# Performance work log

Hardware: AMD Instinct MI355X
Metric: run time of the kernel (lower is better)

Reference implementation:

```python
import jax, jax.numpy as jnp
import numpy as np

H = 8
D_MODEL = 1024
D_K = D_MODEL // H
NEG = -1000000000.0


def layer_norm(x, a, b, eps=1e-06):
    # torch std: unbiased (ddof=1); module divides by (std + eps)
    mean = jnp.mean(x, axis=-1, keepdims=True)
    var = jnp.sum((x - mean) ** 2, axis=-1, keepdims=True) / (x.shape[-1] - 1)
    std = jnp.sqrt(var)
    return a * (x - mean) / (std + eps) + b


def setup_inputs() -> dict:
    key = jax.random.key(0)
    ks = jax.random.split(key, 12)
    B, S, D = 8, 1024, D_MODEL
    inp = {
        "query": jax.random.normal(ks[0], (B, S, D), jnp.float32),
        "value": jax.random.normal(ks[1], (B, S, D), jnp.float32),
        "key": jax.random.normal(ks[2], (B, S, D), jnp.float32),
        "mask": jax.random.randint(ks[3], (B, S), 0, 2, jnp.int32),
        "ln_a": jnp.ones((D,), jnp.float32),
        "ln_b": jnp.zeros((D,), jnp.float32),
        "wq": jax.random.normal(ks[4], (D, D), jnp.float32) * 0.02,
        "bq": jnp.zeros((D,), jnp.float32),
        "wk": jax.random.normal(ks[5], (D, D), jnp.float32) * 0.02,
        "bk": jnp.zeros((D,), jnp.float32),
        "wv": jax.random.normal(ks[6], (D, D), jnp.float32) * 0.02,
        "bv": jnp.zeros((D,), jnp.float32),
        "w_aoa": jax.random.normal(ks[7], (2 * D, 2 * D), jnp.float32) * 0.02,  # [out, in]
        "b_aoa": jnp.zeros((2 * D,), jnp.float32),
    }
    return inp


def reference(query, value, key, mask, ln_a, ln_b, wq, bq, wk, bk, wv, bv, w_aoa, b_aoa):
    B, S, D = query.shape
    # mask [B,S] -> [B,1,1,S]
    m = mask[:, None, None, :]
    # norm_q
    q = layer_norm(query, ln_a, ln_b)
    # QKV projections, split heads -> [B,H,S,Dk]
    def split_heads(x):
        return x.reshape(B, -1, H, D_K).transpose(0, 2, 1, 3)
    q_ = split_heads(q @ wq.T + bq)
    k_ = split_heads(key @ wk.T + bk)
    v_ = split_heads(value @ wv.T + bv)
    scores = jnp.einsum("bhqd,bhkd->bhqk", q_, k_) / jnp.sqrt(jnp.float32(D_K))
    scores = jnp.where(m == 0, NEG, scores)
    p = jax.nn.softmax(scores, axis=-1)
    x = jnp.einsum("bhqk,bhkd->bhqd", p, v_)
    x = x.transpose(0, 2, 1, 3).reshape(B, S, D)
    # AoA: concat with (normed) query, linear to 2D, GLU
    z = jnp.concatenate([x, q], axis=-1) @ w_aoa.T + b_aoa
    a, g = jnp.split(z, 2, axis=-1)
    return a * jax.nn.sigmoid(g)
```

## Files before the change

kernel.cpp:

```cpp
#include <hip/hip_runtime.h>

typedef __attribute__((ext_vector_type(8))) __bf16 bf16x8;
typedef __attribute__((ext_vector_type(4))) float f32x4;
typedef __attribute__((ext_vector_type(16))) float f32x16;
typedef __attribute__((ext_vector_type(2))) int i32x2;

__device__ __forceinline__ ushort f2b(float f) {
    uint u = __builtin_bit_cast(uint, f);
    u += 0x7fffu + ((u >> 16) & 1u);
    return (ushort)(u >> 16);
}
__device__ __forceinline__ float b2f(ushort h) {
    uint u = ((uint)h) << 16;
    return __builtin_bit_cast(float, u);
}
__device__ __forceinline__ uint cvtpk(float a, float b) {
    uint r;
    asm("v_cvt_pk_bf16_f32 %0, %1, %2" : "=v"(r) : "v"(a), "v"(b));
    return r;
}

__global__ __launch_bounds__(256) void cast_kernel(const float* __restrict__ src,
                                                   ushort* __restrict__ dst) {
    size_t i = ((size_t)blockIdx.x * 256 + threadIdx.x) * 4;
    float4 v = *(const float4*)(src + i);
    ushort4 o;
    o.x = f2b(v.x); o.y = f2b(v.y); o.z = f2b(v.z); o.w = f2b(v.w);
    *(ushort4*)(dst + i) = o;
}

__global__ __launch_bounds__(256) void cast_permute_aoa(const float* __restrict__ src,
                                                        ushort* __restrict__ dst) {
    int n1 = blockIdx.x >> 1;
    int c = (blockIdx.x & 1) * 1024 + threadIdx.x * 4;
    int q = ((n1 & 63) | ((n1 >> 7) << 6)) + ((n1 >> 6) & 1) * 1024;
    float4 v = *(const float4*)(src + (size_t)q * 2048 + c);
    ushort4 o;
    o.x = f2b(v.x); o.y = f2b(v.y); o.z = f2b(v.z); o.w = f2b(v.w);
    *(ushort4*)(dst + (size_t)n1 * 2048 + c) = o;
}

__global__ __launch_bounds__(256) void ln_kernel(const float* __restrict__ x,
                                                 const float* __restrict__ ga,
                                                 const float* __restrict__ be,
                                                 ushort* __restrict__ xq) {
    const int row = blockIdx.x, tid = threadIdx.x;
    __shared__ float red[4];
    float4 v = ((const float4*)(x + (size_t)row * 1024))[tid];
    float sm = v.x + v.y + v.z + v.w;
    for (int off = 32; off; off >>= 1) sm += __shfl_xor(sm, off);
    if ((tid & 63) == 0) red[tid >> 6] = sm;
    __syncthreads();
    float mean = (red[0] + red[1] + red[2] + red[3]) * (1.f / 1024.f);
    __syncthreads();
    float dx = v.x - mean, dy = v.y - mean, dz = v.z - mean, dw = v.w - mean;
    float s2 = dx * dx + dy * dy + dz * dz + dw * dw;
    for (int off = 32; off; off >>= 1) s2 += __shfl_xor(s2, off);
    if ((tid & 63) == 0) red[tid >> 6] = s2;
    __syncthreads();
    float var = (red[0] + red[1] + red[2] + red[3]) * (1.f / 1023.f);
    float inv = 1.f / (sqrtf(var) + 1e-6f);
    float4 g = ((const float4*)ga)[tid];
    float4 bb = ((const float4*)be)[tid];
    ushort4 o;
    o.x = f2b(g.x * dx * inv + bb.x);
    o.y = f2b(g.y * dy * inv + bb.y);
    o.z = f2b(g.z * dz * inv + bb.z);
    o.w = f2b(g.w * dw * inv + bb.w);
    *(ushort4*)&xq[(size_t)row * 2048 + 1024 + tid * 4] = o;
}

template <int MODE>
__global__ __launch_bounds__(512, 2) void gemm6(const ushort* __restrict__ Aq, int ldaq,
                                                const ushort* __restrict__ Ak,
                                                const ushort* __restrict__ Av,
                                                const ushort* __restrict__ B, int ldb,
                                                const float* __restrict__ bias0,
                                                const float* __restrict__ bias1,
                                                const float* __restrict__ bias2,
                                                void* __restrict__ out0,
                                                void* __restrict__ out1,
                                                void* __restrict__ out2,
                                                int K, int NB, float qscale) {
    __shared__ ushort lds[2][32768];

    const int tid = threadIdx.x;
    const int w = tid >> 6, l = tid & 63;
    const int wr = w >> 2, wcn = w & 3;
    const int r16 = l & 15, g4 = l >> 4;

    const int bid = blockIdx.x;
    const int cpx = gridDim.x >> 3;
    const int swz = (bid & 7) * cpx + (bid >> 3);
    const int m0 = (swz / NB) * 256;
    const int n0 = (swz % NB) * 256;

    const int region = (MODE == 0) ? (n0 >> 10) : 0;
    const ushort* A = (MODE == 0) ? (region == 0 ? Aq : (region == 1 ? Ak : Av)) : Aq;
    const int lda = (MODE == 0) ? (region == 0 ? ldaq : 1024) : ldaq;

    const int srow8 = l >> 3;
    const int sxor8 = ((l & 7) ^ srow8) * 8;
    const ushort* As0 = A + (size_t)(m0 + w * 8 + srow8) * lda + sxor8;
    const ushort* Bs0 = B + (size_t)(n0 + w * 8 + srow8) * ldb + sxor8;

    f32x4 acc[8][4];
#pragma unroll
    for (int i = 0; i < 8; i++)
#pragma unroll
        for (int j = 0; j < 4; j++) acc[i][j] = (f32x4){0.f, 0.f, 0.f, 0.f};

    const int sw16 = (r16 & 7) << 4;
    char* ldsb = (char*)&lds[0][0];

#define STAGE_H(sel_, HS_, kt_)                                                            \
    do {                                                                                   \
        const int mat_ = (HS_)&1, half_ = (HS_) >> 1;                                      \
        const ushort* sb_ = mat_ ? Bs0 : As0;                                              \
        const int ld_ = mat_ ? ldb : lda;                                                  \
        _Pragma("unroll") for (int li_ = 0; li_ < 2; li_++) {                              \
            const ushort* src_ = sb_ + (size_t)(half_ * 128 + li_ * 64) * ld_ + (kt_)*64;  \
            int dst_ = (sel_)*65536 + mat_ * 32768 + half_ * 16384 + li_ * 8192 + w * 1024;\
            __builtin_amdgcn_global_load_lds(                                              \
                (const __attribute__((address_space(1))) void*)src_,                       \
                (__attribute__((address_space(3))) void*)(ldsb + dst_), 16, 0, 0);         \
        }                                                                                  \
    } while (0)

    auto LDA4 = [&](bf16x8 (&dst)[4][2], int sel, int half) {
#pragma unroll
        for (int ai = 0; ai < 4; ai++)
#pragma unroll
            for (int ks = 0; ks < 2; ks++)
                dst[ai][ks] = *(const bf16x8*)(ldsb + sel * 65536 + half * 16384 +
                                               (wr * 16 + 32 * ai + r16) * 128 +
                                               ((ks * 64 + g4 * 16) ^ sw16));
    };
    auto LDB2 = [&](bf16x8 (&dst)[2][2], int sel, int half) {
#pragma unroll
        for (int bi = 0; bi < 2; bi++)
#pragma unroll
            for (int ks = 0; ks < 2; ks++)
                dst[bi][ks] = *(const bf16x8*)(ldsb + sel * 65536 + 32768 + half * 16384 +
                                               (wcn * 16 + 64 * bi + r16) * 128 +
                                               ((ks * 64 + g4 * 16) ^ sw16));
    };
    auto MM = [&](bf16x8 (&af)[4][2], bf16x8 (&bf)[2][2], int A0, int B0) {
        __builtin_amdgcn_s_setprio(1);
#pragma unroll
        for (int ks = 0; ks < 2; ks++)
#pragma unroll
            for (int ai = 0; ai < 4; ai++)
#pragma unroll
                for (int bi = 0; bi < 2; bi++)
                    acc[A0 + ai][B0 + bi] = __builtin_amdgcn_mfma_f32_16x16x32_bf16(
                        af[ai][ks], bf[bi][ks], acc[A0 + ai][B0 + bi], 0, 0, 0);
        __builtin_amdgcn_s_setprio(0);
    };

    const int NT = K >> 6;

    STAGE_H(0, 0, 0); STAGE_H(0, 1, 0); STAGE_H(0, 2, 0); STAGE_H(0, 3, 0);
    STAGE_H(1, 0, 1); STAGE_H(1, 1, 1); STAGE_H(1, 2, 1);
    asm volatile("s_waitcnt vmcnt(10)" ::: "memory");
    __builtin_amdgcn_s_barrier();

    bf16x8 aL[4][2], aH[4][2], bL[2][2], bH[2][2];

    for (int t = 0; t < NT - 2; ++t) {
        const int sel = t & 1;
        LDA4(aL, sel, 0); LDB2(bL, sel, 0);
        STAGE_H(sel ^ 1, 3, t + 1);
        __builtin_amdgcn_s_barrier();
        MM(aL, bL, 0, 0);
        asm volatile("s_waitcnt vmcnt(10)" ::: "memory");
        __builtin_amdgcn_s_barrier();
        LDA4(aH, sel, 1);
        STAGE_H(sel, 0, t + 2);
        __builtin_amdgcn_s_barrier();
        MM(aH, bL, 4, 0);
        asm volatile("s_waitcnt vmcnt(10)" ::: "memory");
        __builtin_amdgcn_s_barrier();
        LDB2(bH, sel, 1);
        STAGE_H(sel, 1, t + 2);
        __builtin_amdgcn_s_barrier();
        MM(aH, bH, 4, 2);
        __builtin_amdgcn_s_barrier();
        STAGE_H(sel, 2, t + 2);
        __builtin_amdgcn_s_barrier();
        MM(aL, bH, 0, 2);
        asm volatile("s_waitcnt vmcnt(10)" ::: "memory");
        __builtin_amdgcn_s_barrier();
    }
    {
        const int sel = (NT - 2) & 1;
        LDA4(aL, sel, 0); LDB2(bL, sel, 0);
        STAGE_H(sel ^ 1, 3, NT - 1);
        __builtin_amdgcn_s_barrier();
        MM(aL, bL, 0, 0);
        asm volatile("s_waitcnt vmcnt(10)" ::: "memory");
        __builtin_amdgcn_s_barrier();
        LDA4(aH, sel, 1);
        __builtin_amdgcn_s_barrier();
        MM(aH, bL, 4, 0);
        asm volatile("s_waitcnt vmcnt(8)" ::: "memory");
        __builtin_amdgcn_s_barrier();
        LDB2(bH, sel, 1);
        __builtin_amdgcn_s_barrier();
        MM(aH, bH, 4, 2);
        __builtin_amdgcn_s_barrier();
        MM(aL, bH, 0, 2);
        asm volatile("s_waitcnt vmcnt(4)" ::: "memory");
        __builtin_amdgcn_s_barrier();
    }
    {
        const int sel = (NT - 1) & 1;
        LDA4(aL, sel, 0); LDB2(bL, sel, 0);
        __builtin_amdgcn_s_barrier();
        MM(aL, bL, 0, 0);
        asm volatile("s_waitcnt vmcnt(2)" ::: "memory");
        __builtin_amdgcn_s_barrier();
        LDA4(aH, sel, 1);
        __builtin_amdgcn_s_barrier();
        MM(aH, bL, 4, 0);
        asm volatile("s_waitcnt vmcnt(0)" ::: "memory");
        __builtin_amdgcn_s_barrier();
        LDB2(bH, sel, 1);
        MM(aH, bH, 4, 2);
        MM(aL, bH, 0, 2);
    }
#undef STAGE_H

    if (MODE == 1) {
        float* out = (float*)out0;
#pragma unroll
        for (int bp = 0; bp < 2; bp++) {
            int j = (n0 >> 1) + wcn * 16 + 64 * bp + r16;
            float bsa = bias0[j];
            float bsg = bias0[j + 1024];
#pragma unroll
            for (int a_ = 0; a_ < 8; a_++) {
                int mr = m0 + wr * 16 + 32 * a_ + g4 * 4;
#pragma unroll
                for (int r = 0; r < 4; r++) {
                    float av = acc[a_][2 * bp][r] + bsa;
                    float gv = acc[a_][2 * bp + 1][r] + bsg;
                    out[(size_t)(mr + r) * 1024 + j] = av * (1.f / (1.f + __expf(-gv)));
                }
            }
        }
    } else {
        const int nr0 = n0 & 1023;
        const float* bias = region == 0 ? bias0 : (region == 1 ? bias1 : bias2);
        const float scale = region == 0 ? qscale : 1.f;
        if (region < 2) {
            ushort* C = (ushort*)(region == 0 ? out0 : out1);
#pragma unroll
            for (int b_ = 0; b_ < 4; b_++) {
                int n = nr0 + wcn * 16 + 64 * b_ + r16;
                float bs = bias[n];
#pragma unroll
                for (int a_ = 0; a_ < 8; a_++) {
                    int mr = m0 + wr * 16 + 32 * a_ + g4 * 4;
#pragma unroll
                    for (int r = 0; r < 4; r++)
                        C[(size_t)(mr + r) * 1024 + n] = f2b((acc[a_][b_][r] + bs) * scale);
                }
            }
        } else {
            ushort* Vt = (ushort*)out2;
#pragma unroll
            for (int b_ = 0; b_ < 4; b_++) {
                int n = nr0 + wcn * 16 + 64 * b_ + r16;
                float bs = bias[n];
                int h = n >> 7, d = n & 127;
#pragma unroll
                for (int a_ = 0; a_ < 8; a_++) {
                    int mr = m0 + wr * 16 + 32 * a_ + g4 * 4;
                    int bb = mr >> 10, s_ = mr & 1023;
                    ushort4 o;
                    o.x = f2b(acc[a_][b_][0] + bs);
                    o.y = f2b(acc[a_][b_][1] + bs);
                    o.z = f2b(acc[a_][b_][2] + bs);
                    o.w = f2b(acc[a_][b_][3] + bs);
                    *(ushort4*)&Vt[((size_t)(bb * 8 + h) * 128 + d) * 1024 + s_] = o;
                }
            }
        }
    }
}

__global__ __launch_bounds__(256, 2) void attn_kernel(const ushort* __restrict__ Q,
                                                      const ushort* __restrict__ Kt,
                                                      const ushort* __restrict__ Vt,
                                                      const int* __restrict__ mask,
                                                      ushort* __restrict__ xq) {
    __shared__ ushort Ks[2][8192];
    __shared__ ushort Vs[2][8192];

    const int tid = threadIdx.x;
    const int l = tid & 63, wid = tid >> 6;
    const int ql = l & 31, hi = l >> 5;
    const int id = blockIdx.x;
    const int bh = ((id >> 6) << 3) | (id & 7);
    const int qb = (id >> 3) & 7;
    const int b = bh >> 3, h = bh & 7;
    const int q0 = qb * 128 + wid * 32;

    bf16x8 qf[8];
    const ushort* Qrow = Q + (size_t)(b * 1024 + q0 + ql) * 1024 + h * 128 + hi * 8;
#pragma unroll
    for (int ks = 0; ks < 8; ks++) qf[ks] = *(const bf16x8*)(Qrow + ks * 16);

    const ushort* Kg = Kt + ((size_t)b * 1024) * 1024 + h * 128;
    const ushort* Vg = Vt + (size_t)(b * 8 + h) * 128 * 1024;
    const int* mptr = mask + b * 1024;

    f32x16 xacc[4];
#pragma unroll
    for (int i = 0; i < 4; i++)
#pragma unroll
        for (int r = 0; r < 16; r++) xacc[i][r] = 0.f;
    float mrow = -INFINITY, lrow = 0.f, sclp = 0.f;
    bf16x8 pa[4];

    auto STAGE_K = [&](int sel, int t) {
        const int kv0 = t * 64;
#pragma unroll
        for (int it = 0; it < 4; ++it) {
            int ob = it * 4096 + wid * 1024;
            int o = ob + l * 16;
            int row = o >> 8;
            int sc = (o & 255) ^ ((row & 7) << 4);
            const ushort* src = Kg + (size_t)(kv0 + row) * 1024 + (sc >> 1);
            __builtin_amdgcn_global_load_lds((const __attribute__((address_space(1))) void*)src,
                (__attribute__((address_space(3))) void*)((char*)&Ks[sel][0] + ob), 16, 0, 0);
        }
    };
    auto STAGE_V = [&](int sel, int t) {
        const int kv0 = t * 64;
#pragma unroll
        for (int it = 0; it < 4; ++it) {
            int ob = it * 4096 + wid * 1024;
            int o = ob + l * 16;
            int d = o >> 7;
            int sc = (o & 127) ^ ((d & 7) << 4);
            const ushort* src = Vg + (size_t)d * 1024 + kv0 + (sc >> 1);
            __builtin_amdgcn_global_load_lds((const __attribute__((address_space(1))) void*)src,
                (__attribute__((address_space(3))) void*)((char*)&Vs[sel][0] + ob), 16, 0, 0);
        }
    };

    auto QK = [&](f32x16 (&s)[2], int sel, unsigned long long wt) {
        const char* Kb_ = (const char*)&Ks[sel][0];
#pragma unroll
        for (int sub = 0; sub < 2; sub++) {
            f32x16 sacc;
#pragma unroll
            for (int r = 0; r < 16; r++) sacc[r] = 0.f;
            const int rowk = sub * 32 + ql;
            const char* kr = Kb_ + rowk * 256;
            const int sw = (rowk & 7) << 4;
            __builtin_amdgcn_s_setprio(1);
#pragma unroll
            for (int ks = 0; ks < 8; ks++) {
                bf16x8 kfr = *(const bf16x8*)(kr + ((ks * 32 + hi * 16) ^ sw));
                sacc = __builtin_amdgcn_mfma_f32_32x32x16_bf16(kfr, qf[ks], sacc, 0, 0, 0);
            }
            __builtin_amdgcn_s_setprio(0);
#pragma unroll
            for (int q2 = 0; q2 < 4; q2++) {
                uint nib = (uint)(wt >> (8 * q2 + 4 * hi + 32 * sub)) & 15u;
#pragma unroll
                for (int r = 0; r < 4; r++)
                    if (!((nib >> r) & 1u)) sacc[4 * q2 + r] = -1e9f;
            }
            s[sub] = sacc;
        }
    };
    auto PV = [&](int sel) {
        const char* Vb_ = (const char*)&Vs[sel][0];
#pragma unroll
        for (int df = 0; df < 4; df++)
#pragma unroll
            for (int r = 0; r < 16; r++) xacc[df][r] *= sclp;
        __builtin_amdgcn_s_setprio(1);
#pragma unroll
        for (int ks2 = 0; ks2 < 4; ks2++) {
#pragma unroll
            for (int df = 0; df < 4; df++) {
                const int d = df * 32 + ql;
                bf16x8 vfr = *(const bf16x8*)(Vb_ + d * 128 + ((ks2 * 32 + hi * 16) ^ ((d & 7) << 4)));
                xacc[df] = __builtin_amdgcn_mfma_f32_32x32x16_bf16(vfr, pa[ks2], xacc[df], 0, 0, 0);
            }
        }
        __builtin_amdgcn_s_setprio(0);
    };
    auto SOFTMAX = [&](f32x16 (&s)[2]) {
        float pmax = -INFINITY;
#pragma unroll
        for (int res = 0; res < 2; res++)
#pragma unroll
            for (int r = 0; r < 16; r++) pmax = fmaxf(pmax, s[res][r]);
        pmax = fmaxf(pmax, __shfl_xor(pmax, 32));
        float mn = fmaxf(mrow, pmax);
        sclp = __expf(mrow - mn);
        mrow = mn;
        float rsum = 0.f;
#pragma unroll
        for (int res = 0; res < 2; res++)
#pragma unroll
            for (int r = 0; r < 16; r++) {
                float p = __expf(s[res][r] - mn);
                s[res][r] = p;
                rsum += p;
            }
        rsum += __shfl_xor(rsum, 32);
        lrow = lrow * sclp + rsum;
#pragma unroll
        for (int sub = 0; sub < 2; sub++)
#pragma unroll
            for (int g = 0; g < 2; g++) {
                const int b0 = g * 8;
                uint lo01 = cvtpk(s[sub][b0 + 0], s[sub][b0 + 1]);
                uint lo23 = cvtpk(s[sub][b0 + 2], s[sub][b0 + 3]);
                uint hi01 = cvtpk(s[sub][b0 + 4], s[sub][b0 + 5]);
                uint hi23 = cvtpk(s[sub][b0 + 6], s[sub][b0 + 7]);
                i32x2 r02 = __builtin_amdgcn_permlane32_swap((int)lo01, (int)hi01, false, false);
                i32x2 r13 = __builtin_amdgcn_permlane32_swap((int)lo23, (int)hi23, false, false);
                union { bf16x8 v; uint u[4]; } pk;
                pk.u[0] = (uint)r02.x;
                pk.u[1] = (uint)r13.x;
                pk.u[2] = (uint)r02.y;
                pk.u[3] = (uint)r13.y;
                pa[sub * 2 + g] = pk.v;
            }
    };

    STAGE_K(0, 0);
    int mv = mptr[l];
    asm volatile("s_waitcnt vmcnt(0)" ::: "memory");
    __syncthreads();
    STAGE_K(1, 1);
    STAGE_V(0, 0);
    unsigned long long wt = __ballot(mv != 0);
    mv = mptr[64 + l];
    f32x16 s[2];
    QK(s, 0, wt);
    SOFTMAX(s);
    int kc = 1, vc = 0;

    for (int u = 1; u < 16; ++u) {
        wt = __ballot(mv != 0);
        asm volatile("s_waitcnt vmcnt(0)" ::: "memory");
        __syncthreads();
        if (u < 15) STAGE_K(kc ^ 1, u + 1);
        STAGE_V(vc ^ 1, u);
        if (u < 15) mv = mptr[(u + 1) * 64 + l];

        QK(s, kc, wt);
        PV(vc);
        SOFTMAX(s);

        kc ^= 1; vc ^= 1;
    }

    asm volatile("s_waitcnt vmcnt(0)" ::: "memory");
    __syncthreads();
    PV(vc);

    const float inv = 1.f / lrow;
    const size_t orow = (size_t)(b * 1024 + q0 + ql) * 2048 + h * 128;
#pragma unroll
    for (int df = 0; df < 4; df++) {
#pragma unroll
        for (int q2 = 0; q2 < 4; q2++) {
            ushort4 o;
            o.x = f2b(xacc[df][4 * q2 + 0] * inv);
            o.y = f2b(xacc[df][4 * q2 + 1] * inv);
            o.z = f2b(xacc[df][4 * q2 + 2] * inv);
            o.w = f2b(xacc[df][4 * q2 + 3] * inv);
            *(ushort4*)&xq[orow + df * 32 + 8 * q2 + 4 * hi] = o;
        }
    }
}

extern "C" void kernel_launch(void* const* d_in, const int* in_sizes, int n_in,
                              void* d_out, int out_size, void* d_ws, size_t ws_size,
                              hipStream_t stream) {
    const float* query = (const float*)d_in[0];
    const float* value = (const float*)d_in[1];
    const float* key   = (const float*)d_in[2];
    const int*   mask  = (const int*)d_in[3];
    const float* ln_a  = (const float*)d_in[4];
    const float* ln_b  = (const float*)d_in[5];
    const float* wq    = (const float*)d_in[6];
    const float* bq    = (const float*)d_in[7];
    const float* wk    = (const float*)d_in[8];
    const float* bk    = (const float*)d_in[9];
    const float* wv    = (const float*)d_in[10];
    const float* bv    = (const float*)d_in[11];
    const float* waoa  = (const float*)d_in[12];
    const float* baoa  = (const float*)d_in[13];
    float* out = (float*)d_out;

    char* w8 = (char*)d_ws;
    ushort* xq   = (ushort*)(w8);
    ushort* Qb   = (ushort*)(w8 + 33554432);
    ushort* Kb   = (ushort*)(w8 + 50331648);
    ushort* Vt   = (ushort*)(w8 + 67108864);
    ushort* keyb = (ushort*)(w8 + 83886080);
    ushort* valb = (ushort*)(w8 + 100663296);
    ushort* wqb  = (ushort*)(w8 + 117440512);
    ushort* wkb  = (ushort*)(w8 + 119537664);
    ushort* wvb  = (ushort*)(w8 + 121634816);
    ushort* wab  = (ushort*)(w8 + 123731968);

    cast_kernel<<<8192, 256, 0, stream>>>(key, keyb);
    cast_kernel<<<8192, 256, 0, stream>>>(value, valb);
    cast_kernel<<<1024, 256, 0, stream>>>(wq, wqb);
    cast_kernel<<<1024, 256, 0, stream>>>(wk, wkb);
    cast_kernel<<<1024, 256, 0, stream>>>(wv, wvb);
    cast_permute_aoa<<<4096, 256, 0, stream>>>(waoa, wab);
    ln_kernel<<<8192, 256, 0, stream>>>(query, ln_a, ln_b, xq);

    const float qscale = 0.08838834764831845f;

    gemm6<0><<<384, 512, 0, stream>>>(xq + 1024, 2048, keyb, valb,
                                      wqb, 1024, bq, bk, bv,
                                      Qb, Kb, Vt, 1024, 12, qscale);

    attn_kernel<<<512, 256, 0, stream>>>(Qb, Kb, Vt, mask, xq);

    gemm6<1><<<256, 512, 0, stream>>>(xq, 2048, nullptr, nullptr,
                                      wab, 2048, baoa, nullptr, nullptr,
                                      out, nullptr, nullptr, 2048, 8, 1.f);
}
```

Baseline: 232.2 us.

## Use 128x256 tiles for QKV projection GEMM and merge cast launches

Adds a dedicated QKV projection GEMM kernel with 128-row by 256-col tiles and 768 blocks instead of 384 blocks of 256x256, so more CUs are filled on the QKV GEMM. The new kernel has its own pipelined staging schedule sized for the smaller A tile and a smaller LDS footprint. It also merges five cast launches into two by batching key/value and the three weight matrices into contiguous buffers, which cuts launch overhead. The smaller tile lowers per-block data reuse, and the hand-tuned waitcnt counts must match the new load order.

```diff
diff --git a/kernel.cpp b/kernel.cpp
--- a/kernel.cpp
+++ b/kernel.cpp
@@ -20,13 +20,29 @@
     return r;
 }
 
-__global__ __launch_bounds__(256) void cast_kernel(const float* __restrict__ src,
-                                                   ushort* __restrict__ dst) {
-    size_t i = ((size_t)blockIdx.x * 256 + threadIdx.x) * 4;
-    float4 v = *(const float4*)(src + i);
+__global__ __launch_bounds__(256) void cast2_kernel(const float* __restrict__ s0,
+                                                    const float* __restrict__ s1,
+                                                    ushort* __restrict__ dst) {
+    int bid = blockIdx.x;
+    const float* src = (bid < 8192) ? s0 : s1;
+    size_t so = ((size_t)(bid & 8191) * 256 + threadIdx.x) * 4;
+    float4 v = *(const float4*)(src + so);
     ushort4 o;
     o.x = f2b(v.x); o.y = f2b(v.y); o.z = f2b(v.z); o.w = f2b(v.w);
-    *(ushort4*)(dst + i) = o;
+    *(ushort4*)(dst + (size_t)bid * 1024 + threadIdx.x * 4) = o;
+}
+
+__global__ __launch_bounds__(256) void cast3_kernel(const float* __restrict__ s0,
+                                                    const float* __restrict__ s1,
+                                                    const float* __restrict__ s2,
+                                                    ushort* __restrict__ dst) {
+    int bid = blockIdx.x;
+    const float* src = (bid < 1024) ? s0 : ((bid < 2048) ? s1 : s2);
+    size_t so = ((size_t)(bid & 1023) * 256 + threadIdx.x) * 4;
+    float4 v = *(const float4*)(src + so);
+    ushort4 o;
+    o.x = f2b(v.x); o.y = f2b(v.y); o.z = f2b(v.z); o.w = f2b(v.w);
+    *(ushort4*)(dst + (size_t)bid * 1024 + threadIdx.x * 4) = o;
 }
 
 __global__ __launch_bounds__(256) void cast_permute_aoa(const float* __restrict__ src,
@@ -72,16 +88,10 @@
 
 template <int MODE>
 __global__ __launch_bounds__(512, 2) void gemm6(const ushort* __restrict__ Aq, int ldaq,
-                                                const ushort* __restrict__ Ak,
-                                                const ushort* __restrict__ Av,
                                                 const ushort* __restrict__ B, int ldb,
                                                 const float* __restrict__ bias0,
-                                                const float* __restrict__ bias1,
-                                                const float* __restrict__ bias2,
                                                 void* __restrict__ out0,
-                                                void* __restrict__ out1,
-                                                void* __restrict__ out2,
-                                                int K, int NB, float qscale) {
+                                                int K, int NB) {
     __shared__ ushort lds[2][32768];
 
     const int tid = threadIdx.x;
@@ -95,9 +105,8 @@
     const int m0 = (swz / NB) * 256;
     const int n0 = (swz % NB) * 256;
 
-    const int region = (MODE == 0) ? (n0 >> 10) : 0;
-    const ushort* A = (MODE == 0) ? (region == 0 ? Aq : (region == 1 ? Ak : Av)) : Aq;
-    const int lda = (MODE == 0) ? (region == 0 ? ldaq : 1024) : ldaq;
+    const ushort* A = Aq;
+    const int lda = ldaq;
 
     const int srow8 = l >> 3;
     const int sxor8 = ((l & 7) ^ srow8) * 8;
@@ -231,60 +240,217 @@
     }
 #undef STAGE_H
 
-    if (MODE == 1) {
-        float* out = (float*)out0;
-#pragma unroll
-        for (int bp = 0; bp < 2; bp++) {
-            int j = (n0 >> 1) + wcn * 16 + 64 * bp + r16;
-            float bsa = bias0[j];
-            float bsg = bias0[j + 1024];
-#pragma unroll
-            for (int a_ = 0; a_ < 8; a_++) {
+    float* out = (float*)out0;
+#pragma unroll
+    for (int bp = 0; bp < 2; bp++) {
+        int j = (n0 >> 1) + wcn * 16 + 64 * bp + r16;
+        float bsa = bias0[j];
+        float bsg = bias0[j + 1024];
+#pragma unroll
+        for (int a_ = 0; a_ < 8; a_++) {
+            int mr = m0 + wr * 16 + 32 * a_ + g4 * 4;
+#pragma unroll
+            for (int r = 0; r < 4; r++) {
+                float av = acc[a_][2 * bp][r] + bsa;
+                float gv = acc[a_][2 * bp + 1][r] + bsg;
+                out[(size_t)(mr + r) * 1024 + j] = av * (1.f / (1.f + __expf(-gv)));
+            }
+        }
+    }
+}
+
+__global__ __launch_bounds__(512, 2) void gemm7(const ushort* __restrict__ Aq, int ldaq,
+                                                const ushort* __restrict__ Ak,
+                                                const ushort* __restrict__ Av,
+                                                const ushort* __restrict__ B, int ldb,
+                                                const float* __restrict__ bias0,
+                                                const float* __restrict__ bias1,
+                                                const float* __restrict__ bias2,
+                                                ushort* __restrict__ out0,
+                                                ushort* __restrict__ out1,
+                                                ushort* __restrict__ out2,
+                                                float qscale) {
+    __shared__ ushort lds[2][24576];
+
+    const int tid = threadIdx.x;
+    const int w = tid >> 6, l = tid & 63;
+    const int wr = w >> 2, wcn = w & 3;
+    const int r16 = l & 15, g4 = l >> 4;
+
+    const int bid = blockIdx.x;
+    const int cpx = gridDim.x >> 3;
+    const int swz = (bid & 7) * cpx + (bid >> 3);
+    const int m0 = (swz / 12) * 128;
+    const int n0 = (swz % 12) * 256;
+
+    const int region = n0 >> 10;
+    const ushort* A = region == 0 ? Aq : (region == 1 ? Ak : Av);
+    const int lda = region == 0 ? ldaq : 1024;
+
+    const int srow8 = l >> 3;
+    const int sxor8 = ((l & 7) ^ srow8) * 8;
+    const ushort* As0 = A + (size_t)(m0 + w * 8 + srow8) * lda + sxor8;
+    const ushort* Bs0 = B + (size_t)(n0 + w * 8 + srow8) * ldb + sxor8;
+
+    f32x4 acc[4][4];
+#pragma unroll
+    for (int i = 0; i < 4; i++)
+#pragma unroll
+        for (int j = 0; j < 4; j++) acc[i][j] = (f32x4){0.f, 0.f, 0.f, 0.f};
+
+    const int sw16 = (r16 & 7) << 4;
+    char* ldsb = (char*)&lds[0][0];
+
+#define STAGE_A(sel_, h_, kt_)                                                             \
+    __builtin_amdgcn_global_load_lds(                                                      \
+        (const __attribute__((address_space(1))) void*)(As0 + (size_t)((h_)*64) * lda + (kt_)*64), \
+        (__attribute__((address_space(3))) void*)(ldsb + (sel_)*49152 + (h_)*8192 + w * 1024), 16, 0, 0)
+#define STAGE_B(sel_, h_, li_, kt_)                                                        \
+    __builtin_amdgcn_global_load_lds(                                                      \
+        (const __attribute__((address_space(1))) void*)(Bs0 + (size_t)((h_)*128 + (li_)*64) * ldb + (kt_)*64), \
+        (__attribute__((address_space(3))) void*)(ldsb + (sel_)*49152 + 16384 + (h_)*16384 + (li_)*8192 + w * 1024), 16, 0, 0)
+
+    auto LDA2 = [&](bf16x8 (&dst)[2][2], int sel, int half) {
+#pragma unroll
+        for (int ai = 0; ai < 2; ai++)
+#pragma unroll
+            for (int ks = 0; ks < 2; ks++)
+                dst[ai][ks] = *(const bf16x8*)(ldsb + sel * 49152 + half * 8192 +
+                                               (wr * 16 + 32 * ai + r16) * 128 +
+                                               ((ks * 64 + g4 * 16) ^ sw16));
+    };
+    auto LDB2 = [&](bf16x8 (&dst)[2][2], int sel, int half) {
+#pragma unroll
+        for (int bi = 0; bi < 2; bi++)
+#pragma unroll
+            for (int ks = 0; ks < 2; ks++)
+                dst[bi][ks] = *(const bf16x8*)(ldsb + sel * 49152 + 16384 + half * 16384 +
+                                               (wcn * 16 + 64 * bi + r16) * 128 +
+                                               ((ks * 64 + g4 * 16) ^ sw16));
+    };
+    auto MM = [&](bf16x8 (&af)[2][2], bf16x8 (&bf)[2][2], int A0, int B0) {
+        __builtin_amdgcn_s_setprio(1);
+#pragma unroll
+        for (int ks = 0; ks < 2; ks++)
+#pragma unroll
+            for (int ai = 0; ai < 2; ai++)
+#pragma unroll
+                for (int bi = 0; bi < 2; bi++)
+                    acc[A0 + ai][B0 + bi] = __builtin_amdgcn_mfma_f32_16x16x32_bf16(
+                        af[ai][ks], bf[bi][ks], acc[A0 + ai][B0 + bi], 0, 0, 0);
+        __builtin_amdgcn_s_setprio(0);
+    };
+
+    const int NT = 16;
+
+    STAGE_A(0, 0, 0); STAGE_B(0, 0, 0, 0); STAGE_B(0, 0, 1, 0);
+    STAGE_A(0, 1, 0); STAGE_B(0, 1, 0, 0); STAGE_B(0, 1, 1, 0);
+    STAGE_A(1, 0, 1); STAGE_B(1, 0, 0, 1); STAGE_B(1, 0, 1, 1);
+    STAGE_A(1, 1, 1);
+    asm volatile("s_waitcnt vmcnt(7)" ::: "memory");
+    __builtin_amdgcn_s_barrier();
+
+    bf16x8 aL[2][2], aH[2][2], bL[2][2], bH[2][2];
+
+    for (int t = 0; t < NT - 2; ++t) {
+        const int sel = t & 1;
+        LDA2(aL, sel, 0); LDB2(bL, sel, 0);
+        STAGE_B(sel ^ 1, 1, 0, t + 1); STAGE_B(sel ^ 1, 1, 1, t + 1);
+        __builtin_amdgcn_s_barrier();
+        MM(aL, bL, 0, 0);
+        asm volatile("s_waitcnt vmcnt(8)" ::: "memory");
+        __builtin_amdgcn_s_barrier();
+        LDA2(aH, sel, 1);
+        STAGE_A(sel, 0, t + 2);
+        __builtin_amdgcn_s_barrier();
+        MM(aH, bL, 2, 0);
+        asm volatile("s_waitcnt vmcnt(7)" ::: "memory");
+        __builtin_amdgcn_s_barrier();
+        LDB2(bH, sel, 1);
+        STAGE_B(sel, 0, 0, t + 2); STAGE_B(sel, 0, 1, t + 2);
+        __builtin_amdgcn_s_barrier();
+        MM(aH, bH, 2, 2);
+        __builtin_amdgcn_s_barrier();
+        STAGE_A(sel, 1, t + 2);
+        __builtin_amdgcn_s_barrier();
+        MM(aL, bH, 0, 2);
+        asm volatile("s_waitcnt vmcnt(7)" ::: "memory");
+        __builtin_amdgcn_s_barrier();
+    }
+    {
+        const int sel = (NT - 2) & 1;
+        LDA2(aL, sel, 0); LDB2(bL, sel, 0);
+        STAGE_B(sel ^ 1, 1, 0, NT - 1); STAGE_B(sel ^ 1, 1, 1, NT - 1);
+        __builtin_amdgcn_s_barrier();
+        MM(aL, bL, 0, 0);
+        asm volatile("s_waitcnt vmcnt(8)" ::: "memory");
+        __builtin_amdgcn_s_barrier();
+        LDA2(aH, sel, 1);
+        __builtin_amdgcn_s_barrier();
+        MM(aH, bL, 2, 0);
+        asm volatile("s_waitcnt vmcnt(6)" ::: "memory");
+        __builtin_amdgcn_s_barrier();
+        LDB2(bH, sel, 1);
+        __builtin_amdgcn_s_barrier();
+        MM(aH, bH, 2, 2);
+        __builtin_amdgcn_s_barrier();
+        MM(aL, bH, 0, 2);
+        asm volatile("s_waitcnt vmcnt(3)" ::: "memory");
+        __builtin_amdgcn_s_barrier();
+    }
+    {
+        const int sel = (NT - 1) & 1;
+        LDA2(aL, sel, 0); LDB2(bL, sel, 0);
+        __builtin_amdgcn_s_barrier();
+        MM(aL, bL, 0, 0);
+        asm volatile("s_waitcnt vmcnt(2)" ::: "memory");
+        __builtin_amdgcn_s_barrier();
+        LDA2(aH, sel, 1);
+        __builtin_amdgcn_s_barrier();
+        MM(aH, bL, 2, 0);
+        asm volatile("s_waitcnt vmcnt(0)" ::: "memory");
+        __builtin_amdgcn_s_barrier();
+        LDB2(bH, sel, 1);
+        MM(aH, bH, 2, 2);
+        MM(aL, bH, 0, 2);
+    }
+#undef STAGE_A
+#undef STAGE_B
+
+    const int nr0 = n0 & 1023;
+    const float* bias = region == 0 ? bias0 : (region == 1 ? bias1 : bias2);
+    const float scale = region == 0 ? qscale : 1.f;
+    if (region < 2) {
+        ushort* C = region == 0 ? out0 : out1;
+#pragma unroll
+        for (int b_ = 0; b_ < 4; b_++) {
+            int n = nr0 + wcn * 16 + 64 * b_ + r16;
+            float bs = bias[n];
+#pragma unroll
+            for (int a_ = 0; a_ < 4; a_++) {
                 int mr = m0 + wr * 16 + 32 * a_ + g4 * 4;
 #pragma unroll
-                for (int r = 0; r < 4; r++) {
-                    float av = acc[a_][2 * bp][r] + bsa;
-                    float gv = acc[a_][2 * bp + 1][r] + bsg;
-                    out[(size_t)(mr + r) * 1024 + j] = av * (1.f / (1.f + __expf(-gv)));
-                }
+                for (int r = 0; r < 4; r++)
+                    C[(size_t)(mr + r) * 1024 + n] = f2b((acc[a_][b_][r] + bs) * scale);
             }
         }
     } else {
-        const int nr0 = n0 & 1023;
-        const float* bias = region == 0 ? bias0 : (region == 1 ? bias1 : bias2);
-        const float scale = region == 0 ? qscale : 1.f;
-        if (region < 2) {
-            ushort* C = (ushort*)(region == 0 ? out0 : out1);
-#pragma unroll
-            for (int b_ = 0; b_ < 4; b_++) {
-                int n = nr0 + wcn * 16 + 64 * b_ + r16;
-                float bs = bias[n];
-#pragma unroll
-                for (int a_ = 0; a_ < 8; a_++) {
-                    int mr = m0 + wr * 16 + 32 * a_ + g4 * 4;
-#pragma unroll
-                    for (int r = 0; r < 4; r++)
-                        C[(size_t)(mr + r) * 1024 + n] = f2b((acc[a_][b_][r] + bs) * scale);
-                }
-            }
-        } else {
-            ushort* Vt = (ushort*)out2;
-#pragma unroll
-            for (int b_ = 0; b_ < 4; b_++) {
-                int n = nr0 + wcn * 16 + 64 * b_ + r16;
-                float bs = bias[n];
-                int h = n >> 7, d = n & 127;
-#pragma unroll
-                for (int a_ = 0; a_ < 8; a_++) {
-                    int mr = m0 + wr * 16 + 32 * a_ + g4 * 4;
-                    int bb = mr >> 10, s_ = mr & 1023;
-                    ushort4 o;
-                    o.x = f2b(acc[a_][b_][0] + bs);
-                    o.y = f2b(acc[a_][b_][1] + bs);
-                    o.z = f2b(acc[a_][b_][2] + bs);
-                    o.w = f2b(acc[a_][b_][3] + bs);
-                    *(ushort4*)&Vt[((size_t)(bb * 8 + h) * 128 + d) * 1024 + s_] = o;
-                }
+        ushort* Vt = out2;
+#pragma unroll
+        for (int b_ = 0; b_ < 4; b_++) {
+            int n = nr0 + wcn * 16 + 64 * b_ + r16;
+            float bs = bias[n];
+            int h = n >> 7, d = n & 127;
+#pragma unroll
+            for (int a_ = 0; a_ < 4; a_++) {
+                int mr = m0 + wr * 16 + 32 * a_ + g4 * 4;
+                int bb = mr >> 10, s_ = mr & 1023;
+                ushort4 o;
+                o.x = f2b(acc[a_][b_][0] + bs);
+                o.y = f2b(acc[a_][b_][1] + bs);
+                o.z = f2b(acc[a_][b_][2] + bs);
+                o.w = f2b(acc[a_][b_][3] + bs);
+                *(ushort4*)&Vt[((size_t)(bb * 8 + h) * 128 + d) * 1024 + s_] = o;
             }
         }
     }
@@ -510,29 +676,22 @@
     ushort* Kb   = (ushort*)(w8 + 50331648);
     ushort* Vt   = (ushort*)(w8 + 67108864);
     ushort* keyb = (ushort*)(w8 + 83886080);
-    ushort* valb = (ushort*)(w8 + 100663296);
     ushort* wqb  = (ushort*)(w8 + 117440512);
-    ushort* wkb  = (ushort*)(w8 + 119537664);
-    ushort* wvb  = (ushort*)(w8 + 121634816);
     ushort* wab  = (ushort*)(w8 + 123731968);
 
-    cast_kernel<<<8192, 256, 0, stream>>>(key, keyb);
-    cast_kernel<<<8192, 256, 0, stream>>>(value, valb);
-    cast_kernel<<<1024, 256, 0, stream>>>(wq, wqb);
-    cast_kernel<<<1024, 256, 0, stream>>>(wk, wkb);
-    cast_kernel<<<1024, 256, 0, stream>>>(wv, wvb);
+    cast2_kernel<<<16384, 256, 0, stream>>>(key, value, keyb);
+    cast3_kernel<<<3072, 256, 0, stream>>>(wq, wk, wv, wqb);
     cast_permute_aoa<<<4096, 256, 0, stream>>>(waoa, wab);
     ln_kernel<<<8192, 256, 0, stream>>>(query, ln_a, ln_b, xq);
 
     const float qscale = 0.08838834764831845f;
-
-    gemm6<0><<<384, 512, 0, stream>>>(xq + 1024, 2048, keyb, valb,
-                                      wqb, 1024, bq, bk, bv,
-                                      Qb, Kb, Vt, 1024, 12, qscale);
+    ushort* valb = keyb + 8388608;
+
+    gemm7<<<768, 512, 0, stream>>>(xq + 1024, 2048, keyb, valb,
+                                   wqb, 1024, bq, bk, bv,
+                                   Qb, Kb, Vt, qscale);
 
     attn_kernel<<<512, 256, 0, stream>>>(Qb, Kb, Vt, mask, xq);
 
-    gemm6<1><<<256, 512, 0, stream>>>(xq, 2048, nullptr, nullptr,
-                                      wab, 2048, baoa, nullptr, nullptr,
-                                      out, nullptr, nullptr, 2048, 8, 1.f);
-}
+    gemm6<1><<<256, 512, 0, stream>>>(xq, 2048, wab, 2048, baoa, out, 2048, 8);
+}
```

Result: no change. 228.0 us (-1.8%).
